# Kernel tuning notes

Measured on AMD Instinct MI355X. Metric: run time of the kernel, lower is better.

## Reference

```python
import jax, jax.numpy as jnp
from jax import lax
import numpy as np

H, W, C = 2160, 3840, 3
CROP = 3  # rows trimmed top and bottom before filtering


def median1d(x, size, axis):
    """Sliding-window median along `axis` with edge padding (matches
    np.pad(mode='edge') + centered window + np.median for odd size)."""
    pad = size // 2
    pw = [(0, 0)] * x.ndim
    pw[axis] = (pad, pad)
    xp = jnp.pad(x, pw, mode='edge')
    n = x.shape[axis]
    # stack the `size` shifted views -> (..., size), median = middle of sort
    windows = jnp.stack(
        [lax.slice_in_dim(xp, i, i + n, axis=axis) for i in range(size)], axis=-1)
    return jnp.sort(windows, axis=-1)[..., size // 2]


def shift1(x, axis):
    """np.pad(x,(1,0),'constant')[:-1] along `axis`: shift forward, zero-fill."""
    pw = [(0, 0)] * x.ndim
    pw[axis] = (1, 0)
    return lax.slice_in_dim(jnp.pad(x, pw), 0, x.shape[axis], axis=axis)


def setup_inputs() -> dict:
    key = jax.random.key(0)
    k1, k2 = jax.random.split(key)
    img = jax.random.normal(k1, (H, W, C), dtype=jnp.float32)
    mask = jax.random.randint(k2, (H, W), 0, 2, dtype=jnp.int32)
    return {"img": img, "mask": mask, "vertical_size": 5}


def reference(img, mask, vertical_size):
    # mask is read but unused by the original module's math.
    x = img[CROP:-CROP]                       # (H-6, W, C)
    # vertical pass: median(v), shift down 1, median(3) along rows
    v = median1d(x, vertical_size, axis=0)
    v = median1d(shift1(v, axis=0), 3, axis=0)
    # horizontal pass (original reuses vertical_size here): along columns
    h = median1d(v, vertical_size, axis=1)
    h = median1d(shift1(h, axis=1), 3, axis=1)
    return h
```

## Files before the change

kernel.cpp:

```cpp
#include <hip/hip_runtime.h>

#define HH    2160
#define WW    3840
#define CROPC 3
#define NN    (HH - 2*CROPC)
#define WFLAT (WW * 3)

constexpr int TY    = 16;
constexpr int TXF   = 192;
constexpr int SX    = TXF + 18;
constexpr int NTH   = 256;
constexpr int TPR   = 16;
constexpr int XROWS = TY + 6;

constexpr int PSTR  = 76;
constexpr int PLANE = TY * PSTR + 8;

__device__ __forceinline__ float med3f(float a, float b, float c) {
    return fmaxf(fminf(a, b), fminf(fmaxf(a, b), c));
}
__device__ __forceinline__ float med5f(float a, float b, float c, float d, float e) {
    float t;
    t = fminf(a, b); b = fmaxf(a, b); a = t;
    t = fminf(c, d); d = fmaxf(c, d); c = t;
    t = fminf(a, c); c = fmaxf(a, c); a = t;
    t = fminf(b, d); d = fmaxf(b, d); b = t;
    t = fminf(b, c); c = fmaxf(b, c); b = t;
    return fminf(c, fmaxf(b, e));
}

__global__ __launch_bounds__(NTH, 8) void fused_median(const float* __restrict__ img,
                                                       float* __restrict__ out) {
    __shared__ float v2s[3 * PLANE];

    const int tid = threadIdx.x;
    const int r0 = blockIdx.y * TY;
    const int f0 = blockIdx.x * TXF;

    if (tid < SX) {
        const int ch   = tid % 3;
        const int pcol = tid / 3;
        const int cc   = min(max(f0 / 3 - 4 + pcol, 0), WW - 1);
        const float* colp = img + (size_t)CROPC * WFLAT + (cc * 3 + ch);

        float xv[XROWS];
        #pragma unroll
        for (int i = 0; i < XROWS; ++i) {
            const int rr = min(max(r0 - 4 + i, 0), NN - 1);
            xv[i] = colp[(size_t)rr * WFLAT];
        }
        __builtin_amdgcn_sched_barrier(0);

        float vm2 = 0.f, vm1 = 0.f;
        #pragma unroll
        for (int i = 4; i < XROWS; ++i) {
            const float vc = med5f(xv[i-4], xv[i-3], xv[i-2], xv[i-1], xv[i]);
            if (i >= 6) {
                const int rz = r0 + i - 6;
                float a = vm2, b = vm1;
                if (rz == NN - 1) a = b;
                if (rz == 1)      a = 0.f;
                if (rz == 0)    { a = 0.f; b = 0.f; }
                v2s[ch * PLANE + (i - 6) * PSTR + pcol] = med3f(a, b, vc);
            }
            vm2 = vm1; vm1 = vc;
        }
    }
    __syncthreads();

    const int lr    = tid >> 4;
    const int kk    = tid & (TPR - 1);
    const int r_out = r0 + lr;
    if (r_out >= NN) return;

    const int cbase = f0 / 3 + 4 * kk;
    const bool edge = (cbase <= 1) || (cbase + 3 >= WW - 1);

    float o[12];
    #pragma unroll
    for (int c = 0; c < 3; ++c) {
        const float* pb = &v2s[c * PLANE + lr * PSTR + 4 * kk];
        const float4 q0 = *(const float4*)(pb);
        const float4 q1 = *(const float4*)(pb + 4);
        const float4 q2 = *(const float4*)(pb + 8);
        const float ss[12] = {q0.x,q0.y,q0.z,q0.w, q1.x,q1.y,q1.z,q1.w,
                              q2.x,q2.y,q2.z,q2.w};
        float h[6];
        #pragma unroll
        for (int m = 0; m < 6; ++m)
            h[m] = med5f(ss[m], ss[m+1], ss[m+2], ss[m+3], ss[m+4]);
        if (!edge) {
            #pragma unroll
            for (int n = 0; n < 4; ++n)
                o[3*n + c] = med3f(h[n], h[n+1], h[n+2]);
        } else {
            #pragma unroll
            for (int n = 0; n < 4; ++n) {
                const int ci = cbase + n;
                float A = h[n], B = h[n+1];
                if (ci == WW - 1) A = B;
                if (ci == 1)      A = 0.f;
                if (ci == 0)    { A = 0.f; B = 0.f; }
                o[3*n + c] = med3f(A, B, h[n+2]);
            }
        }
    }

    float4* op = (float4*)(out + (size_t)r_out * WFLAT + f0 + 12 * kk);
    #pragma unroll
    for (int q = 0; q < 3; ++q)
        op[q] = make_float4(o[4*q], o[4*q+1], o[4*q+2], o[4*q+3]);
}

extern "C" void kernel_launch(void* const* d_in, const int* in_sizes, int n_in,
                              void* d_out, int out_size, void* d_ws, size_t ws_size,
                              hipStream_t stream) {
    const float* img = (const float*)d_in[0];
    float* out = (float*)d_out;
    dim3 grid(WFLAT / TXF, (NN + TY - 1) / TY);
    fused_median<<<grid, NTH, 0, stream>>>(img, out);
}
```

Measured before the change: 49.15 us.

## Process 64-row bands per block with sliding window and double-buffered loads

Each block now walks a 64-row band in four 16-row chunks instead of handling one 16-row tile. It carries the vertical median window and previous values across chunks, which removes the 6-row halo reload and recompute at every tile. The next chunk's rows are prefetched into a register double buffer while the current chunk is processed. In exchange there are more __syncthreads per block, higher register pressure (launch bounds lowered to 7), and a quarter as many blocks, which may reduce parallelism.

Measured after the change: 69.62 us. 41.7% more time.

```diff
diff --git a/kernel.cpp b/kernel.cpp
--- a/kernel.cpp
+++ b/kernel.cpp
@@ -6,15 +6,15 @@
 #define NN    (HH - 2*CROPC)
 #define WFLAT (WW * 3)
 
-constexpr int TY    = 16;
+constexpr int BAND  = 64;
+constexpr int CHNK  = 16;
+constexpr int NIT   = BAND / CHNK;
 constexpr int TXF   = 192;
 constexpr int SX    = TXF + 18;
 constexpr int NTH   = 256;
-constexpr int TPR   = 16;
-constexpr int XROWS = TY + 6;
 
 constexpr int PSTR  = 76;
-constexpr int PLANE = TY * PSTR + 8;
+constexpr int PLANE = CHNK * PSTR + 8;
 
 __device__ __forceinline__ float med3f(float a, float b, float c) {
     return fmaxf(fminf(a, b), fminf(fmaxf(a, b), c));
@@ -29,87 +29,111 @@
     return fminf(c, fmaxf(b, e));
 }
 
-__global__ __launch_bounds__(NTH, 8) void fused_median(const float* __restrict__ img,
+__global__ __launch_bounds__(NTH, 7) void fused_median(const float* __restrict__ img,
                                                        float* __restrict__ out) {
     __shared__ float v2s[3 * PLANE];
 
     const int tid = threadIdx.x;
-    const int r0 = blockIdx.y * TY;
+    const int r0 = blockIdx.y * BAND;
     const int f0 = blockIdx.x * TXF;
 
-    if (tid < SX) {
-        const int ch   = tid % 3;
-        const int pcol = tid / 3;
-        const int cc   = min(max(f0 / 3 - 4 + pcol, 0), WW - 1);
-        const float* colp = img + (size_t)CROPC * WFLAT + (cc * 3 + ch);
+    const bool p1   = (tid < SX);
+    const int  ch   = tid % 3;
+    const int  pcol = tid / 3;
+    const int  cc   = min(max(f0 / 3 - 4 + pcol, 0), WW - 1);
+    const float* colp = img + (size_t)CROPC * WFLAT + (cc * 3 + ch);
 
-        float xv[XROWS];
+    const int lr    = tid >> 4;
+    const int kk    = tid & 15;
+    const int cbase = f0 / 3 + 4 * kk;
+    const bool edge2 = (cbase <= 1) || (cbase + 3 >= WW - 1);
+
+    float xw0, xw1, xw2, xw3, vm2, vm1;
+    float buf[2][CHNK];
+
+    if (p1) {
+        float p[6];
         #pragma unroll
-        for (int i = 0; i < XROWS; ++i) {
+        for (int i = 0; i < 6; ++i) {
             const int rr = min(max(r0 - 4 + i, 0), NN - 1);
-            xv[i] = colp[(size_t)rr * WFLAT];
+            p[i] = colp[(size_t)rr * WFLAT];
         }
-        __builtin_amdgcn_sched_barrier(0);
+        #pragma unroll
+        for (int i = 0; i < CHNK; ++i) {
+            const int rr = min(r0 + 2 + i, NN - 1);
+            buf[0][i] = colp[(size_t)rr * WFLAT];
+        }
+        vm2 = med5f(p[0], p[1], p[2], p[3], p[4]);
+        vm1 = med5f(p[1], p[2], p[3], p[4], p[5]);
+        xw0 = p[2]; xw1 = p[3]; xw2 = p[4]; xw3 = p[5];
+    }
 
-        float vm2 = 0.f, vm1 = 0.f;
-        #pragma unroll
-        for (int i = 4; i < XROWS; ++i) {
-            const float vc = med5f(xv[i-4], xv[i-3], xv[i-2], xv[i-1], xv[i]);
-            if (i >= 6) {
-                const int rz = r0 + i - 6;
+    #pragma unroll
+    for (int k = 0; k < NIT; ++k) {
+        const int Rk = r0 + CHNK * k;
+
+        if (p1) {
+            if (k < NIT - 1) {
+                #pragma unroll
+                for (int i = 0; i < CHNK; ++i) {
+                    const int rr = min(Rk + CHNK + 2 + i, NN - 1);
+                    buf[(k & 1) ^ 1][i] = colp[(size_t)rr * WFLAT];
+                }
+            }
+            #pragma unroll
+            for (int j = 0; j < CHNK; ++j) {
+                const float xn = buf[k & 1][j];
+                const float vc = med5f(xw0, xw1, xw2, xw3, xn);
+                const int rz = Rk + j;
                 float a = vm2, b = vm1;
                 if (rz == NN - 1) a = b;
                 if (rz == 1)      a = 0.f;
                 if (rz == 0)    { a = 0.f; b = 0.f; }
-                v2s[ch * PLANE + (i - 6) * PSTR + pcol] = med3f(a, b, vc);
-            }
-            vm2 = vm1; vm1 = vc;
-        }
-    }
-    __syncthreads();
-
-    const int lr    = tid >> 4;
-    const int kk    = tid & (TPR - 1);
-    const int r_out = r0 + lr;
-    if (r_out >= NN) return;
-
-    const int cbase = f0 / 3 + 4 * kk;
-    const bool edge = (cbase <= 1) || (cbase + 3 >= WW - 1);
-
-    float o[12];
-    #pragma unroll
-    for (int c = 0; c < 3; ++c) {
-        const float* pb = &v2s[c * PLANE + lr * PSTR + 4 * kk];
-        const float4 q0 = *(const float4*)(pb);
-        const float4 q1 = *(const float4*)(pb + 4);
-        const float4 q2 = *(const float4*)(pb + 8);
-        const float ss[12] = {q0.x,q0.y,q0.z,q0.w, q1.x,q1.y,q1.z,q1.w,
-                              q2.x,q2.y,q2.z,q2.w};
-        float h[6];
-        #pragma unroll
-        for (int m = 0; m < 6; ++m)
-            h[m] = med5f(ss[m], ss[m+1], ss[m+2], ss[m+3], ss[m+4]);
-        if (!edge) {
-            #pragma unroll
-            for (int n = 0; n < 4; ++n)
-                o[3*n + c] = med3f(h[n], h[n+1], h[n+2]);
-        } else {
-            #pragma unroll
-            for (int n = 0; n < 4; ++n) {
-                const int ci = cbase + n;
-                float A = h[n], B = h[n+1];
-                if (ci == WW - 1) A = B;
-                if (ci == 1)      A = 0.f;
-                if (ci == 0)    { A = 0.f; B = 0.f; }
-                o[3*n + c] = med3f(A, B, h[n+2]);
+                v2s[ch * PLANE + j * PSTR + pcol] = med3f(a, b, vc);
+                xw0 = xw1; xw1 = xw2; xw2 = xw3; xw3 = xn;
+                vm2 = vm1; vm1 = vc;
             }
         }
+        __syncthreads();
+
+        const int r_out = Rk + lr;
+        if (r_out < NN) {
+            float o[12];
+            #pragma unroll
+            for (int c = 0; c < 3; ++c) {
+                const float* pb = &v2s[c * PLANE + lr * PSTR + 4 * kk];
+                const float4 q0 = *(const float4*)(pb);
+                const float4 q1 = *(const float4*)(pb + 4);
+                const float2 q2 = *(const float2*)(pb + 8);
+                const float ss[10] = {q0.x,q0.y,q0.z,q0.w, q1.x,q1.y,q1.z,q1.w,
+                                      q2.x,q2.y};
+                float h[6];
+                #pragma unroll
+                for (int m = 0; m < 6; ++m)
+                    h[m] = med5f(ss[m], ss[m+1], ss[m+2], ss[m+3], ss[m+4]);
+                if (!edge2) {
+                    #pragma unroll
+                    for (int n = 0; n < 4; ++n)
+                        o[3*n + c] = med3f(h[n], h[n+1], h[n+2]);
+                } else {
+                    #pragma unroll
+                    for (int n = 0; n < 4; ++n) {
+                        const int ci = cbase + n;
+                        float A = h[n], B = h[n+1];
+                        if (ci == WW - 1) A = B;
+                        if (ci == 1)      A = 0.f;
+                        if (ci == 0)    { A = 0.f; B = 0.f; }
+                        o[3*n + c] = med3f(A, B, h[n+2]);
+                    }
+                }
+            }
+            float4* op = (float4*)(out + (size_t)r_out * WFLAT + f0 + 12 * kk);
+            op[0] = make_float4(o[0], o[1], o[2],  o[3]);
+            op[1] = make_float4(o[4], o[5], o[6],  o[7]);
+            op[2] = make_float4(o[8], o[9], o[10], o[11]);
+        }
+        __syncthreads();
     }
-
-    float4* op = (float4*)(out + (size_t)r_out * WFLAT + f0 + 12 * kk);
-    #pragma unroll
-    for (int q = 0; q < 3; ++q)
-        op[q] = make_float4(o[4*q], o[4*q+1], o[4*q+2], o[4*q+3]);
 }
 
 extern "C" void kernel_launch(void* const* d_in, const int* in_sizes, int n_in,
@@ -117,6 +141,6 @@
                               hipStream_t stream) {
     const float* img = (const float*)d_in[0];
     float* out = (float*)d_out;
-    dim3 grid(WFLAT / TXF, (NN + TY - 1) / TY);
+    dim3 grid(WFLAT / TXF, (NN + BAND - 1) / BAND);
     fused_median<<<grid, NTH, 0, stream>>>(img, out);
 }
```
